# Kernel tuning notes

Hardware: AMD Instinct MI355X
Metric: run time of the kernel (lower is better)

The kernel has to match this reference:

```python
import jax, jax.numpy as jnp
import numpy as np

NUM_HEADS = 16
ROPE_BASE = 10000.0


def _rope_cos_sin(seq_len, head_dim, dtype):
    inv_freq = 1.0 / (ROPE_BASE ** (jnp.arange(0, head_dim, 2, dtype=jnp.float32) / head_dim))
    t = jnp.arange(seq_len, dtype=jnp.float32)
    freqs = t[:, None] * inv_freq[None, :]          # [S, hd/2]
    emb = jnp.concatenate([freqs, freqs], axis=-1)  # [S, hd]
    return jnp.cos(emb).astype(dtype), jnp.sin(emb).astype(dtype)


def _rotate_half(x):
    x1, x2 = jnp.split(x, 2, axis=-1)
    return jnp.concatenate([-x2, x1], axis=-1)


def setup_inputs() -> dict:
    key = jax.random.key(0)
    ks = jax.random.split(key, 5)
    B, S, D = 2, 2048, 2048
    x = jax.random.normal(ks[0], (B, S, D), dtype=jnp.float32)
    Wq = jax.random.normal(ks[1], (D, D), dtype=jnp.float32) * (D ** -0.5)
    Wk = jax.random.normal(ks[2], (D, D), dtype=jnp.float32) * (D ** -0.5)
    Wv = jax.random.normal(ks[3], (D, D), dtype=jnp.float32) * (D ** -0.5)
    Wo = jax.random.normal(ks[4], (D, D), dtype=jnp.float32) * (D ** -0.5)
    return {"x": x, "Wq": Wq, "Wk": Wk, "Wv": Wv, "Wo": Wo}


def reference(x, Wq, Wk, Wv, Wo):
    B, S, D = x.shape
    H = NUM_HEADS
    hd = D // H
    scale = hd ** -0.5
    # Linear(bias=False): y = x @ W.T ; reshape to [B, H, S, hd]
    def proj(W):
        return jnp.einsum('bsd,ed->bse', x, W).reshape(B, S, H, hd).transpose(0, 2, 1, 3)
    q, k, v = proj(Wq), proj(Wk), proj(Wv)
    cos, sin = _rope_cos_sin(S, hd, x.dtype)  # [S, hd]
    cos = cos[None, None, :, :]
    sin = sin[None, None, :, :]
    q = q * cos + _rotate_half(q) * sin
    k = k * cos + _rotate_half(k) * sin
    scores = jnp.einsum('bhqd,bhkd->bhqk', q, k) * scale  # [B,H,S,S]
    causal = jnp.triu(jnp.ones((S, S), dtype=bool), k=1)
    scores = jnp.where(causal[None, None], jnp.finfo(scores.dtype).min, scores)
    attn = jax.nn.softmax(scores, axis=-1)
    out = jnp.einsum('bhqk,bhkd->bhqd', attn, v)  # [B,H,S,hd]
    out = out.transpose(0, 2, 1, 3).reshape(B, S, D)
    return jnp.einsum('bsd,ed->bse', out, Wo)
```

## Files before the change

kernel.cpp:

```cpp
#include <hip/hip_runtime.h>
#include <hip/hip_bf16.h>
#include <math.h>

typedef __bf16 bf16_t;
typedef __attribute__((ext_vector_type(8))) __bf16 bf16x8;
typedef __attribute__((ext_vector_type(4))) float f32x4;
typedef __attribute__((ext_vector_type(16))) float f32x16;

#define S_LEN 2048
#define DM    2048
#define NH    16
#define HD    128
#define MTOT  4096

__device__ inline float finz(float v) {
    return (v == v && fabsf(v) < 1e30f) ? v : 0.f;
}

__device__ inline void gload_lds16(const bf16_t* g, bf16_t* l) {
    __builtin_amdgcn_global_load_lds(
        (const __attribute__((address_space(1))) void*)g,
        (__attribute__((address_space(3))) void*)l, 16, 0, 0);
}

__device__ __forceinline__ int crow4(int g, int hi) {
    return (g & 3) + ((g >> 2) << 3) + (hi << 2);
}
__device__ __forceinline__ unsigned pk2(float x, float y) {
    union { bf16_t h; unsigned short u; } a, b;
    a.h = (bf16_t)x; b.h = (bf16_t)y;
    return (unsigned)a.u | ((unsigned)b.u << 16);
}
__device__ __forceinline__ bf16x8 pack4(unsigned w0, unsigned w1, unsigned w2, unsigned w3) {
    union { unsigned w[4]; bf16x8 v; } u;
    u.w[0] = w0; u.w[1] = w1; u.w[2] = w2; u.w[3] = w3;
    return u.v;
}

#define MFMA32(a, b, c) __builtin_amdgcn_mfma_f32_32x32x16_bf16(a, b, c, 0, 0, 0)

__global__ __launch_bounds__(256)
void dtype_probe(const unsigned short* __restrict__ p, unsigned int* __restrict__ flag)
{
    __shared__ int tot;
    if (threadIdx.x == 0) tot = 0;
    __syncthreads();
    int weird = 0;
    for (int i = threadIdx.x; i < 4096; i += 256) {
        unsigned short u = p[2*i];
        int e = (u >> 7) & 0xFF;
        if (e >= 0xC8 || (e != 0 && e <= 0x38)) weird++;
    }
    atomicAdd(&tot, weird);
    __syncthreads();
    if (threadIdx.x == 0) *flag = (tot > 512) ? 1u : 0u;
}

__global__ __launch_bounds__(256)
void convert_in(const void* __restrict__ src, bf16_t* __restrict__ dst, int n,
                const unsigned int* __restrict__ flag)
{
    const bool f32 = (*flag != 0);
    int i = (blockIdx.x*256 + threadIdx.x)*4;
    if (i + 3 >= n) return;
    if (f32) {
        const float4 v = *(const float4*)((const float*)src + i);
        dst[i  ] = (bf16_t)v.x; dst[i+1] = (bf16_t)v.y;
        dst[i+2] = (bf16_t)v.z; dst[i+3] = (bf16_t)v.w;
    } else {
        *(uint2*)(dst + i) = *(const uint2*)((const bf16_t*)src + i);
    }
}

template<int MODE>
__global__ __launch_bounds__(256)
void gemm_bt(const bf16_t* __restrict__ A, const bf16_t* __restrict__ W,
             void* __restrict__ Cv)
{
    __shared__ bf16_t As[128*64];
    __shared__ bf16_t Ws[128*64];

    const int t    = threadIdx.x;
    const int wv   = t >> 6;
    const int lane = t & 63;
    const int c16  = lane & 15;
    const int quad = lane >> 4;
    const int wm   = wv & 1;
    const int wn   = wv >> 1;
    const int mb   = blockIdx.x;
    const int nb   = blockIdx.y;
    const int c7   = c16 & 7;

    const int srow = lane >> 3;
    const int sphy = (lane & 7) ^ srow;
    const bf16_t* Ab = A + (size_t)(mb*128 + wv*32 + srow)*DM + sphy*8;
    const bf16_t* Wb = W + (size_t)(nb*128 + wv*32 + srow)*DM + sphy*8;

    f32x4 acc[4][4];
    #pragma unroll
    for (int i = 0; i < 4; ++i)
        #pragma unroll
        for (int j = 0; j < 4; ++j)
            acc[i][j] = (f32x4){0.f, 0.f, 0.f, 0.f};

    for (int kb = 0; kb < DM/64; ++kb) {
        __syncthreads();
        #pragma unroll
        for (int i = 0; i < 4; ++i) {
            gload_lds16(Ab + (size_t)kb*64 + (size_t)i*8*DM, As + (wv*32 + i*8)*64);
            gload_lds16(Wb + (size_t)kb*64 + (size_t)i*8*DM, Ws + (wv*32 + i*8)*64);
        }
        __syncthreads();

        #pragma unroll
        for (int kk = 0; kk < 2; ++kk) {
            const int ph = ((kk*4 + quad) ^ c7) * 8;
            bf16x8 af[4], bfr[4];
            #pragma unroll
            for (int mt = 0; mt < 4; ++mt)
                af[mt] = *(const bf16x8*)(As + (wm*64 + mt*16 + c16)*64 + ph);
            #pragma unroll
            for (int nt = 0; nt < 4; ++nt)
                bfr[nt] = *(const bf16x8*)(Ws + (nt*32 + wn*16 + c16)*64 + ph);
            #pragma unroll
            for (int mt = 0; mt < 4; ++mt)
                #pragma unroll
                for (int nt = 0; nt < 4; ++nt)
                    acc[mt][nt] = __builtin_amdgcn_mfma_f32_16x16x32_bf16(
                                      af[mt], bfr[nt], acc[mt][nt], 0, 0, 0);
        }
    }

    #pragma unroll
    for (int mt = 0; mt < 4; ++mt) {
        #pragma unroll
        for (int r = 0; r < 4; ++r) {
            const int m = mb*128 + wm*64 + mt*16 + quad*4 + r;
            if (MODE == 2) {
                bf16_t* C = (bf16_t*)Cv;
                size_t base = (size_t)m*DM + nb*128;
                #pragma unroll
                for (int nt = 0; nt < 4; ++nt)
                    C[base + nt*32 + wn*16 + c16] = (bf16_t)finz(acc[mt][nt][r]);
            } else if (MODE == 3) {
                float* C = (float*)Cv;
                size_t base = (size_t)m*DM + nb*128;
                #pragma unroll
                for (int nt = 0; nt < 4; ++nt)
                    C[base + nt*32 + wn*16 + c16] = finz(acc[mt][nt][r]);
            } else {
                const int g  = nb >> 4;
                const int hh = nb & 15;
                bf16_t* C = (bf16_t*)Cv + (size_t)g * MTOT * DM;
                const int b = m >> 11;
                const int s = m & (S_LEN - 1);
                size_t base = ((size_t)(b*NH + hh)*S_LEN + s)*HD;
                if (g == 2) {
                    #pragma unroll
                    for (int nt = 0; nt < 4; ++nt)
                        C[base + nt*32 + wn*16 + c16] = (bf16_t)finz(acc[mt][nt][r]);
                } else {
                    #pragma unroll
                    for (int nt = 0; nt < 2; ++nt) {
                        int t64 = nt*32 + wn*16 + c16;
                        float invf = exp2f(-(float)t64 * 0.20762050593046014f);
                        float ang  = (float)s * invf;
                        float sn, cs;
                        sincosf(ang, &sn, &cs);
                        float lo  = acc[mt][nt  ][r];
                        float hi2 = acc[mt][nt+2][r];
                        C[base + t64     ] = (bf16_t)finz(lo*cs - hi2*sn);
                        C[base + t64 + 64] = (bf16_t)finz(hi2*cs + lo*sn);
                    }
                }
            }
        }
    }
}

__global__ __launch_bounds__(256)
void transpose_v(const bf16_t* __restrict__ Vb, bf16_t* __restrict__ VT)
{
    __shared__ bf16_t Lt[64*72];
    const int t  = threadIdx.x;
    const int st = blockIdx.x;
    const int dt = blockIdx.y;
    const int bh = blockIdx.z;
    #pragma unroll
    for (int i = 0; i < 2; ++i) {
        int ch = t + i*256;
        int sr = ch >> 3, c = ch & 7;
        *(uint4*)(Lt + sr*72 + c*8) =
            *(const uint4*)(Vb + ((size_t)bh*S_LEN + st*64 + sr)*HD + dt*64 + c*8);
    }
    __syncthreads();
    #pragma unroll
    for (int i = 0; i < 2; ++i) {
        int ch = t + i*256;
        int dr = ch >> 3, c = ch & 7;
        bf16x8 v;
        #pragma unroll
        for (int j = 0; j < 8; ++j) v[j] = Lt[(c*8 + j)*72 + dr];
        *(bf16x8*)(VT + ((size_t)bh*HD + dt*64 + dr)*S_LEN + st*64 + c*8) = v;
    }
}

__global__ __launch_bounds__(512, 2)
void flash_attn(const bf16_t* __restrict__ Q, const bf16_t* __restrict__ K,
                const bf16_t* __restrict__ VT, bf16_t* __restrict__ O)
{
    __shared__ bf16_t Ks[64*128];
    __shared__ bf16_t Vs[128*64];
    __shared__ float  Ocmb[4][32*128];
    __shared__ float  lcmb[4][32];

    const int t    = threadIdx.x;
    const int wid  = t >> 6;
    const int lane = t & 63;
    const int qw   = wid & 3;
    const int kh   = wid >> 2;
    const int c32  = lane & 31;
    const int hi   = lane >> 5;
    const int ix   = blockIdx.x;
    const int bh   = blockIdx.y;

    const float scale = 0.08838834764831845f;
    const float SMAX  = 12.0f;

    bf16x8 onesf;
    #pragma unroll
    for (int j = 0; j < 8; ++j) onesf[j] = (bf16_t)1.0f;

    for (int pass = 0; pass < 2; ++pass) {
        const int Qt   = pass ? (15 - ix) : ix;
        const int qt0  = Qt * 128;
        const int qrow = qt0 + qw*32 + c32;
        const int qmin = qt0 + qw*32;

        bf16x8 qf[8];
        {
            const bf16_t* qp = Q + ((size_t)bh*S_LEN + qrow)*HD;
            #pragma unroll
            for (int s = 0; s < 8; ++s)
                qf[s] = *(const bf16x8*)(qp + s*16 + hi*8);
        }

        f32x16 oacc[4];
        f32x16 lacc;
        #pragma unroll
        for (int e = 0; e < 16; ++e) lacc[e] = 0.f;
        #pragma unroll
        for (int dt = 0; dt < 4; ++dt)
            #pragma unroll
            for (int e = 0; e < 16; ++e) oacc[dt][e] = 0.f;

        const int ktend = 2*Qt + 1;
        for (int kt = 0; kt <= ktend; ++kt) {
            __syncthreads();
            #pragma unroll
            for (int j = 0; j < 2; ++j) {
                int base = wid*8 + j*4;
                int rg   = base + (lane >> 4);
                int ph   = (lane & 15) ^ (rg & 7);
                gload_lds16(K + ((size_t)bh*S_LEN + kt*64 + rg)*HD + ph*8,
                            Ks + base*128);
            }
            #pragma unroll
            for (int j = 0; j < 2; ++j) {
                int base = wid*16 + j*8;
                int rg   = base + (lane >> 3);
                int ph   = (lane & 7) ^ (rg & 7);
                gload_lds16(VT + ((size_t)bh*HD + rg)*S_LEN + kt*64 + ph*8,
                            Vs + base*64);
            }
            __syncthreads();

            const int kbase = kt*64 + kh*32;
            if (kbase > qmin + 31) continue;

            f32x16 sacc;
            #pragma unroll
            for (int e = 0; e < 16; ++e) sacc[e] = 0.f;
            const int krow = kh*32 + c32;
            const int ksw  = krow & 7;
            #pragma unroll
            for (int s = 0; s < 8; ++s) {
                bf16x8 kf = *(const bf16x8*)(Ks + krow*128 + (((s*2 + hi) ^ ksw) << 3));
                sacc = MFMA32(kf, qf[s], sacc);
            }

            float p[16];
            if (kbase + 31 > qmin) {
                #pragma unroll
                for (int g = 0; g < 16; ++g) {
                    int kg = kbase + crow4(g, hi);
                    p[g] = (kg <= qrow) ? __expf(sacc[g]*scale - SMAX) : 0.f;
                }
            } else {
                #pragma unroll
                for (int g = 0; g < 16; ++g)
                    p[g] = __expf(sacc[g]*scale - SMAX);
            }

            unsigned a0 = pk2(p[0],  p[1]),  b0 = pk2(p[2],  p[3]);
            unsigned a1 = pk2(p[4],  p[5]),  b1 = pk2(p[6],  p[7]);
            unsigned a2 = pk2(p[8],  p[9]),  b2 = pk2(p[10], p[11]);
            unsigned a3 = pk2(p[12], p[13]), b3 = pk2(p[14], p[15]);
            asm volatile("v_permlane32_swap_b32 %0, %1" : "+v"(a0), "+v"(a1));
            asm volatile("v_permlane32_swap_b32 %0, %1" : "+v"(b0), "+v"(b1));
            asm volatile("v_permlane32_swap_b32 %0, %1" : "+v"(a2), "+v"(a3));
            asm volatile("v_permlane32_swap_b32 %0, %1" : "+v"(b2), "+v"(b3));
            bf16x8 pa0 = pack4(a0, b0, a1, b1);
            bf16x8 pa1 = pack4(a2, b2, a3, b3);

            lacc = MFMA32(pa0, onesf, lacc);
            lacc = MFMA32(pa1, onesf, lacc);
            const int ks0 = kh*2 + 0, ks1 = kh*2 + 1;
            #pragma unroll
            for (int dt = 0; dt < 4; ++dt) {
                const int vrow = dt*32 + c32;
                const int vsw  = vrow & 7;
                bf16x8 vf0 = *(const bf16x8*)(Vs + vrow*64 + (((ks0*2 + hi) ^ vsw) << 3));
                oacc[dt] = MFMA32(pa0, vf0, oacc[dt]);
                bf16x8 vf1 = *(const bf16x8*)(Vs + vrow*64 + (((ks1*2 + hi) ^ vsw) << 3));
                oacc[dt] = MFMA32(pa1, vf1, oacc[dt]);
            }
        }

        if (kh == 1) {
            #pragma unroll
            for (int g = 0; g < 16; ++g) {
                int ql = crow4(g, hi);
                #pragma unroll
                for (int dt = 0; dt < 4; ++dt)
                    Ocmb[qw][ql*128 + dt*32 + c32] = oacc[dt][g];
            }
            if (c32 == 0) {
                #pragma unroll
                for (int g = 0; g < 16; ++g)
                    lcmb[qw][crow4(g, hi)] = lacc[g];
            }
        }
        __syncthreads();
        if (kh == 0) {
            const int b = bh >> 4, h = bh & 15;
            #pragma unroll
            for (int g = 0; g < 16; ++g) {
                int ql = crow4(g, hi);
                int qg = qt0 + qw*32 + ql;
                float lt = lacc[g] + lcmb[qw][ql];
                float rl = 1.0f / fmaxf(lt, 1e-37f);
                #pragma unroll
                for (int dt = 0; dt < 4; ++dt) {
                    float v = oacc[dt][g] + Ocmb[qw][ql*128 + dt*32 + c32];
                    O[((size_t)(b*S_LEN + qg))*DM + h*HD + dt*32 + c32] =
                        (bf16_t)finz(v*rl);
                }
            }
        }
    }
}

extern "C" void kernel_launch(void* const* d_in, const int* in_sizes, int n_in,
                              void* d_out, int out_size, void* d_ws, size_t ws_size,
                              hipStream_t stream)
{
    const void* x_raw  = d_in[0];
    const void* Wq_raw = d_in[1];
    const void* Wk_raw = d_in[2];
    const void* Wv_raw = d_in[3];
    const void* Wo_raw = d_in[4];

    const int NX = MTOT*DM;
    const int NW = DM*DM;

    unsigned int* flag = (unsigned int*)d_ws;
    bf16_t* xb  = (bf16_t*)((char*)d_ws + 16);
    bf16_t* Wqb = xb  + NX;
    bf16_t* Wkb = Wqb + NW;
    bf16_t* Wvb = Wkb + NW;
    bf16_t* Wob = Wvb + NW;
    bf16_t* Qb  = Wob + NW;
    bf16_t* Kb  = Qb + NX;
    bf16_t* Vb  = Kb + NX;
    bf16_t* Ob  = Vb + NX;
    bf16_t* VT  = xb;

    bool out_is_f32 = true;
    {
        void* base = nullptr; size_t sz = 0;
        if (hipMemGetAddressRange((hipDeviceptr_t*)&base, &sz,
                                  (hipDeviceptr_t)d_out) == hipSuccess && sz != 0) {
            if (sz < (size_t)out_size * 3) out_is_f32 = false;
        }
    }

    dim3 bb(256);
    hipLaunchKernelGGL(dtype_probe, dim3(1), bb, 0, stream,
                       (const unsigned short*)x_raw, flag);
    hipLaunchKernelGGL(convert_in, dim3(NX/1024), bb, 0, stream, x_raw,  xb,  NX, flag);
    hipLaunchKernelGGL(convert_in, dim3(NW/1024), bb, 0, stream, Wq_raw, Wqb, NW, flag);
    hipLaunchKernelGGL(convert_in, dim3(NW/1024), bb, 0, stream, Wk_raw, Wkb, NW, flag);
    hipLaunchKernelGGL(convert_in, dim3(NW/1024), bb, 0, stream, Wv_raw, Wvb, NW, flag);
    hipLaunchKernelGGL(convert_in, dim3(NW/1024), bb, 0, stream, Wo_raw, Wob, NW, flag);

    hipLaunchKernelGGL((gemm_bt<4>), dim3(32, 48), bb, 0, stream, xb, Wqb, (void*)Qb);
    hipLaunchKernelGGL(transpose_v, dim3(32, 2, 32), bb, 0, stream, Vb, VT);
    hipLaunchKernelGGL(flash_attn, dim3(8, 32), dim3(512), 0, stream, Qb, Kb, VT, Ob);
    if (out_is_f32)
        hipLaunchKernelGGL((gemm_bt<3>), dim3(32, 16), bb, 0, stream, Ob, Wob, d_out);
    else
        hipLaunchKernelGGL((gemm_bt<2>), dim3(32, 16), bb, 0, stream, Ob, Wob, d_out);
}
```

Baseline: 417.9 us.

## Replace GEMM with 256x256 double-buffered 8-wave kernel and precomputed RoPE table

The 128x128 single-buffered projection GEMM becomes a 256x256-tile, 512-thread kernel. It double-buffers LDS via global_load_lds, splits the MFMA work into phases separated by barriers, and raises priority with setprio to overlap loads with compute. RoPE sin/cos now comes from a precomputed table instead of per-element sincosf. The four weight conversions are merged into one launch. Larger tiles cut global traffic per FLOP, but each block uses 128KB of LDS and many more registers, and the output GEMM launches only 128 blocks, which could underfill the GPU.

Measured after the change: 458.0 us. 1.1x slower.

```diff
diff --git a/kernel.cpp b/kernel.cpp
--- a/kernel.cpp
+++ b/kernel.cpp
@@ -23,6 +23,12 @@
         (__attribute__((address_space(3))) void*)l, 16, 0, 0);
 }
 
+__device__ __forceinline__ void phb() {
+    __builtin_amdgcn_sched_barrier(0);
+    __builtin_amdgcn_s_barrier();
+    __builtin_amdgcn_sched_barrier(0);
+}
+
 __device__ __forceinline__ int crow4(int g, int hi) {
     return (g & 3) + ((g >> 2) << 3) + (hi << 2);
 }
@@ -37,6 +43,7 @@
     return u.v;
 }
 
+#define MFMA16(a, b, c) __builtin_amdgcn_mfma_f32_16x16x32_bf16(a, b, c, 0, 0, 0)
 #define MFMA32(a, b, c) __builtin_amdgcn_mfma_f32_32x32x16_bf16(a, b, c, 0, 0, 0)
 
 __global__ __launch_bounds__(256)
@@ -72,105 +79,208 @@
     }
 }
 
+__global__ __launch_bounds__(256)
+void convert_w4(const void* __restrict__ s0, const void* __restrict__ s1,
+                const void* __restrict__ s2, const void* __restrict__ s3,
+                bf16_t* __restrict__ dst, const unsigned int* __restrict__ flag)
+{
+    const bool f32 = (*flag != 0);
+    const void* src = (blockIdx.y == 0) ? s0 : (blockIdx.y == 1) ? s1
+                    : (blockIdx.y == 2) ? s2 : s3;
+    bf16_t* d = dst + (size_t)blockIdx.y * DM * DM;
+    int i = (blockIdx.x*256 + threadIdx.x)*4;
+    if (f32) {
+        const float4 v = *(const float4*)((const float*)src + i);
+        d[i  ] = (bf16_t)v.x; d[i+1] = (bf16_t)v.y;
+        d[i+2] = (bf16_t)v.z; d[i+3] = (bf16_t)v.w;
+    } else {
+        *(uint2*)(d + i) = *(const uint2*)((const bf16_t*)src + i);
+    }
+}
+
+__global__ __launch_bounds__(256)
+void rope_table(float2* __restrict__ tab)
+{
+    int i = blockIdx.x*256 + threadIdx.x;
+    int s = i >> 6, t64 = i & 63;
+    float invf = exp2f(-(float)t64 * 0.20762050593046014f);
+    float ang  = (float)s * invf;
+    float sn, cs;
+    sincosf(ang, &sn, &cs);
+    tab[i] = make_float2(cs, sn);
+}
+
 template<int MODE>
-__global__ __launch_bounds__(256)
-void gemm_bt(const bf16_t* __restrict__ A, const bf16_t* __restrict__ W,
-             void* __restrict__ Cv)
-{
-    __shared__ bf16_t As[128*64];
-    __shared__ bf16_t Ws[128*64];
+__global__ __launch_bounds__(512, 2)
+void gemm8(const bf16_t* __restrict__ A, const bf16_t* __restrict__ W,
+           void* __restrict__ Cv, const float2* __restrict__ rtab)
+{
+    __shared__ bf16_t Ls[2][2][256*64];
 
     const int t    = threadIdx.x;
-    const int wv   = t >> 6;
+    const int wid  = t >> 6;
     const int lane = t & 63;
     const int c16  = lane & 15;
     const int quad = lane >> 4;
-    const int wm   = wv & 1;
-    const int wn   = wv >> 1;
+    const int wm   = wid >> 2;
+    const int wn   = wid & 3;
     const int mb   = blockIdx.x;
     const int nb   = blockIdx.y;
-    const int c7   = c16 & 7;
 
     const int srow = lane >> 3;
-    const int sphy = (lane & 7) ^ srow;
-    const bf16_t* Ab = A + (size_t)(mb*128 + wv*32 + srow)*DM + sphy*8;
-    const bf16_t* Wb = W + (size_t)(nb*128 + wv*32 + srow)*DM + sphy*8;
-
-    f32x4 acc[4][4];
+    const int sch  = (lane & 7) ^ srow;
+    const bf16_t* Ab = A + (size_t)(mb*256 + wid*32 + srow)*DM + sch*8;
+    const bf16_t* Wb = W + (size_t)(nb*256 + wid*32 + srow)*DM + sch*8;
+
+    auto stage = [&](int buf, int kt) {
+        const size_t koff = (size_t)kt*64;
+        #pragma unroll
+        for (int j = 0; j < 4; ++j)
+            gload_lds16(Ab + koff + (size_t)j*8*DM, &Ls[buf][0][(wid*32 + j*8)*64]);
+        #pragma unroll
+        for (int j = 0; j < 4; ++j)
+            gload_lds16(Wb + koff + (size_t)j*8*DM, &Ls[buf][1][(wid*32 + j*8)*64]);
+    };
+    auto rdA = [&](int buf, int qm, int i, int kk) -> bf16x8 {
+        int row = wm*128 + qm*64 + i*16 + c16;
+        int ch  = (kk*4 + quad) ^ (row & 7);
+        return *(const bf16x8*)&Ls[buf][0][row*64 + ch*8];
+    };
+    auto rdB = [&](int buf, int k, int kk) -> bf16x8 {
+        int row = wn*16 + k*64 + c16;
+        int ch  = (kk*4 + quad) ^ (row & 7);
+        return *(const bf16x8*)&Ls[buf][1][row*64 + ch*8];
+    };
+
+    f32x4 acc[8][4];
     #pragma unroll
-    for (int i = 0; i < 4; ++i)
+    for (int i = 0; i < 8; ++i)
         #pragma unroll
         for (int j = 0; j < 4; ++j)
             acc[i][j] = (f32x4){0.f, 0.f, 0.f, 0.f};
 
-    for (int kb = 0; kb < DM/64; ++kb) {
-        __syncthreads();
+    stage(0, 0);
+    stage(1, 1);
+    asm volatile("s_waitcnt vmcnt(8)" ::: "memory");
+    __builtin_amdgcn_s_barrier();
+
+    const int NT = DM/64;
+    #pragma unroll 2
+    for (int kt = 0; kt < NT; ++kt) {
+        const int b = kt & 1;
+        bf16x8 af[4][2], bf0[2][2], bf1[2][2];
+
         #pragma unroll
         for (int i = 0; i < 4; ++i) {
-            gload_lds16(Ab + (size_t)kb*64 + (size_t)i*8*DM, As + (wv*32 + i*8)*64);
-            gload_lds16(Wb + (size_t)kb*64 + (size_t)i*8*DM, Ws + (wv*32 + i*8)*64);
-        }
-        __syncthreads();
-
-        #pragma unroll
-        for (int kk = 0; kk < 2; ++kk) {
-            const int ph = ((kk*4 + quad) ^ c7) * 8;
-            bf16x8 af[4], bfr[4];
-            #pragma unroll
-            for (int mt = 0; mt < 4; ++mt)
-                af[mt] = *(const bf16x8*)(As + (wm*64 + mt*16 + c16)*64 + ph);
-            #pragma unroll
-            for (int nt = 0; nt < 4; ++nt)
-                bfr[nt] = *(const bf16x8*)(Ws + (nt*32 + wn*16 + c16)*64 + ph);
-            #pragma unroll
-            for (int mt = 0; mt < 4; ++mt)
-                #pragma unroll
-                for (int nt = 0; nt < 4; ++nt)
-                    acc[mt][nt] = __builtin_amdgcn_mfma_f32_16x16x32_bf16(
-                                      af[mt], bfr[nt], acc[mt][nt], 0, 0, 0);
-        }
+            af[i][0] = rdA(b, 0, i, 0); af[i][1] = rdA(b, 0, i, 1);
+        }
+        #pragma unroll
+        for (int jj = 0; jj < 2; ++jj) {
+            bf0[jj][0] = rdB(b, jj, 0); bf0[jj][1] = rdB(b, jj, 1);
+        }
+        phb();
+        __builtin_amdgcn_s_setprio(1);
+        #pragma unroll
+        for (int kk = 0; kk < 2; ++kk)
+            #pragma unroll
+            for (int i = 0; i < 4; ++i)
+                #pragma unroll
+                for (int jj = 0; jj < 2; ++jj)
+                    acc[i][jj] = MFMA16(af[i][kk], bf0[jj][kk], acc[i][jj]);
+        __builtin_amdgcn_s_setprio(0);
+        phb();
+
+        #pragma unroll
+        for (int jj = 0; jj < 2; ++jj) {
+            bf1[jj][0] = rdB(b, 2+jj, 0); bf1[jj][1] = rdB(b, 2+jj, 1);
+        }
+        phb();
+        __builtin_amdgcn_s_setprio(1);
+        #pragma unroll
+        for (int kk = 0; kk < 2; ++kk)
+            #pragma unroll
+            for (int i = 0; i < 4; ++i)
+                #pragma unroll
+                for (int jj = 0; jj < 2; ++jj)
+                    acc[i][2+jj] = MFMA16(af[i][kk], bf1[jj][kk], acc[i][2+jj]);
+        __builtin_amdgcn_s_setprio(0);
+        phb();
+
+        #pragma unroll
+        for (int i = 0; i < 4; ++i) {
+            af[i][0] = rdA(b, 1, i, 0); af[i][1] = rdA(b, 1, i, 1);
+        }
+        phb();
+        __builtin_amdgcn_s_setprio(1);
+        #pragma unroll
+        for (int kk = 0; kk < 2; ++kk)
+            #pragma unroll
+            for (int i = 0; i < 4; ++i)
+                #pragma unroll
+                for (int jj = 0; jj < 2; ++jj)
+                    acc[4+i][jj] = MFMA16(af[i][kk], bf0[jj][kk], acc[4+i][jj]);
+        __builtin_amdgcn_s_setprio(0);
+        phb();
+
+        __builtin_amdgcn_s_setprio(1);
+        #pragma unroll
+        for (int kk = 0; kk < 2; ++kk)
+            #pragma unroll
+            for (int i = 0; i < 4; ++i)
+                #pragma unroll
+                for (int jj = 0; jj < 2; ++jj)
+                    acc[4+i][2+jj] = MFMA16(af[i][kk], bf1[jj][kk], acc[4+i][2+jj]);
+        __builtin_amdgcn_s_setprio(0);
+        phb();
+
+        if (kt + 2 < NT) {
+            stage(b, kt + 2);
+            asm volatile("s_waitcnt vmcnt(8)" ::: "memory");
+        } else {
+            asm volatile("s_waitcnt vmcnt(0)" ::: "memory");
+        }
+        __builtin_amdgcn_s_barrier();
+        __builtin_amdgcn_sched_barrier(0);
     }
 
     #pragma unroll
-    for (int mt = 0; mt < 4; ++mt) {
+    for (int mi = 0; mi < 8; ++mi) {
         #pragma unroll
         for (int r = 0; r < 4; ++r) {
-            const int m = mb*128 + wm*64 + mt*16 + quad*4 + r;
+            const int m = mb*256 + wm*128 + mi*16 + quad*4 + r;
             if (MODE == 2) {
                 bf16_t* C = (bf16_t*)Cv;
-                size_t base = (size_t)m*DM + nb*128;
-                #pragma unroll
-                for (int nt = 0; nt < 4; ++nt)
-                    C[base + nt*32 + wn*16 + c16] = (bf16_t)finz(acc[mt][nt][r]);
+                #pragma unroll
+                for (int k = 0; k < 4; ++k)
+                    C[(size_t)m*DM + nb*256 + wn*16 + k*64 + c16] =
+                        (bf16_t)finz(acc[mi][k][r]);
             } else if (MODE == 3) {
                 float* C = (float*)Cv;
-                size_t base = (size_t)m*DM + nb*128;
-                #pragma unroll
-                for (int nt = 0; nt < 4; ++nt)
-                    C[base + nt*32 + wn*16 + c16] = finz(acc[mt][nt][r]);
+                #pragma unroll
+                for (int k = 0; k < 4; ++k)
+                    C[(size_t)m*DM + nb*256 + wn*16 + k*64 + c16] =
+                        finz(acc[mi][k][r]);
             } else {
-                const int g  = nb >> 4;
-                const int hh = nb & 15;
-                bf16_t* C = (bf16_t*)Cv + (size_t)g * MTOT * DM;
-                const int b = m >> 11;
-                const int s = m & (S_LEN - 1);
-                size_t base = ((size_t)(b*NH + hh)*S_LEN + s)*HD;
-                if (g == 2) {
-                    #pragma unroll
-                    for (int nt = 0; nt < 4; ++nt)
-                        C[base + nt*32 + wn*16 + c16] = (bf16_t)finz(acc[mt][nt][r]);
-                } else {
-                    #pragma unroll
-                    for (int nt = 0; nt < 2; ++nt) {
-                        int t64 = nt*32 + wn*16 + c16;
-                        float invf = exp2f(-(float)t64 * 0.20762050593046014f);
-                        float ang  = (float)s * invf;
-                        float sn, cs;
-                        sincosf(ang, &sn, &cs);
-                        float lo  = acc[mt][nt  ][r];
-                        float hi2 = acc[mt][nt+2][r];
-                        C[base + t64     ] = (bf16_t)finz(lo*cs - hi2*sn);
-                        C[base + t64 + 64] = (bf16_t)finz(hi2*cs + lo*sn);
+                const int s  = m & (S_LEN - 1);
+                const int bb = m >> 11;
+                #pragma unroll
+                for (int hp = 0; hp < 2; ++hp) {
+                    const int n   = nb*256 + wn*16 + c16 + hp*128;
+                    const int g   = n >> 11;
+                    const int e   = n & (DM - 1);
+                    const int hh  = e >> 7;
+                    const int t64 = e & 63;
+                    bf16_t* C = (bf16_t*)Cv + (size_t)g * MTOT * DM;
+                    size_t base = ((size_t)(bb*NH + hh)*S_LEN + s)*HD;
+                    float lo  = acc[mi][2*hp  ][r];
+                    float hi2 = acc[mi][2*hp+1][r];
+                    if (g == 2) {
+                        C[base + t64     ] = (bf16_t)finz(lo);
+                        C[base + t64 + 64] = (bf16_t)finz(hi2);
+                    } else {
+                        float2 cs2 = rtab[s*64 + t64];
+                        C[base + t64     ] = (bf16_t)finz(lo*cs2.x - hi2*cs2.y);
+                        C[base + t64 + 64] = (bf16_t)finz(hi2*cs2.x + lo*cs2.y);
                     }
                 }
             }
@@ -384,6 +494,7 @@
     bf16_t* Kb  = Qb + NX;
     bf16_t* Vb  = Kb + NX;
     bf16_t* Ob  = Vb + NX;
+    float2* rtab = (float2*)(Ob + NX);
     bf16_t* VT  = xb;
 
     bool out_is_f32 = true;
@@ -398,17 +509,19 @@
     dim3 bb(256);
     hipLaunchKernelGGL(dtype_probe, dim3(1), bb, 0, stream,
                        (const unsigned short*)x_raw, flag);
-    hipLaunchKernelGGL(convert_in, dim3(NX/1024), bb, 0, stream, x_raw,  xb,  NX, flag);
-    hipLaunchKernelGGL(convert_in, dim3(NW/1024), bb, 0, stream, Wq_raw, Wqb, NW, flag);
-    hipLaunchKernelGGL(convert_in, dim3(NW/1024), bb, 0, stream, Wk_raw, Wkb, NW, flag);
-    hipLaunchKernelGGL(convert_in, dim3(NW/1024), bb, 0, stream, Wv_raw, Wvb, NW, flag);
-    hipLaunchKernelGGL(convert_in, dim3(NW/1024), bb, 0, stream, Wo_raw, Wob, NW, flag);
-
-    hipLaunchKernelGGL((gemm_bt<4>), dim3(32, 48), bb, 0, stream, xb, Wqb, (void*)Qb);
+    hipLaunchKernelGGL(convert_in, dim3(NX/1024), bb, 0, stream, x_raw, xb, NX, flag);
+    hipLaunchKernelGGL(convert_w4, dim3(NW/1024, 4), bb, 0, stream,
+                       Wq_raw, Wk_raw, Wv_raw, Wo_raw, Wqb, flag);
+    hipLaunchKernelGGL(rope_table, dim3(S_LEN*64/256), bb, 0, stream, rtab);
+
+    hipLaunchKernelGGL((gemm8<4>), dim3(16, 24), dim3(512), 0, stream,
+                       xb, Wqb, (void*)Qb, rtab);
     hipLaunchKernelGGL(transpose_v, dim3(32, 2, 32), bb, 0, stream, Vb, VT);
     hipLaunchKernelGGL(flash_attn, dim3(8, 32), dim3(512), 0, stream, Qb, Kb, VT, Ob);
     if (out_is_f32)
-        hipLaunchKernelGGL((gemm_bt<3>), dim3(32, 16), bb, 0, stream, Ob, Wob, d_out);
+        hipLaunchKernelGGL((gemm8<3>), dim3(16, 8), dim3(512), 0, stream,
+                           Ob, Wob, d_out, rtab);
     else
-        hipLaunchKernelGGL((gemm_bt<2>), dim3(32, 16), bb, 0, stream, Ob, Wob, d_out);
-}
+        hipLaunchKernelGGL((gemm8<2>), dim3(16, 8), dim3(512), 0, stream,
+                           Ob, Wob, d_out, rtab);
+}
```
